# Performance work log

Hardware: AMD Instinct MI355X
Metric: run time of the kernel (lower is better)

## Reference

```python
import jax, jax.numpy as jnp
import numpy as np

EPS_GN = 1e-8
EPS_ATTN = 1e-8


def setup_inputs() -> dict:
    key = jax.random.key(0)
    ks = jax.random.split(key, 13)
    B, C, N = 4, 512, 2048
    s = 0.02
    return {
        "x": jax.random.normal(ks[0], (B, C, N), jnp.float32),
        "dw_w": jax.random.normal(ks[1], (C, 3), jnp.float32) * s,
        "pw_w": jax.random.normal(ks[2], (C, C), jnp.float32) * s,
        "u_w": jax.random.normal(ks[3], (2 * C, C), jnp.float32) * s,
        "u_b": jax.random.normal(ks[4], (2 * C,), jnp.float32) * s,
        "v_w": jax.random.normal(ks[5], (2 * C, C), jnp.float32) * s,
        "v_b": jax.random.normal(ks[6], (2 * C,), jnp.float32) * s,
        "h_w": jax.random.normal(ks[7], (C, C), jnp.float32) * s,
        "h_b": jax.random.normal(ks[8], (C,), jnp.float32) * s,
        "q_w": jax.random.normal(ks[9], (C, C), jnp.float32) * s,
        "k_w": jax.random.normal(ks[10], (C, C), jnp.float32) * s,
        "o_w": jax.random.normal(ks[11], (C, 2 * C), jnp.float32) * s,
        "o_b": jax.random.normal(ks[12], (C,), jnp.float32) * s,
    }


def reference(x, dw_w, pw_w, u_w, u_b, v_w, v_b, h_w, h_b, q_w, k_w, o_w, o_b):
    # x: [B, C, N]
    C = x.shape[1]
    # GroupNorm(1, C): normalize over (C, N) per sample; affine is identity-init
    # in torch but we follow the module math with default weight=1, bias=0
    mean = jnp.mean(x, axis=(1, 2), keepdims=True)
    var = jnp.var(x, axis=(1, 2), keepdims=True)
    z = (x - mean) * jax.lax.rsqrt(var + EPS_GN)

    # local depthwise conv k=3, pad=1 (cross-correlation), no bias
    zp = jnp.pad(z, ((0, 0), (0, 0), (1, 1)))
    dw = (dw_w[:, 0, None] * zp[:, :, :-2]
          + dw_w[:, 1, None] * zp[:, :, 1:-1]
          + dw_w[:, 2, None] * zp[:, :, 2:])
    # pointwise conv (no bias)
    z = z + jnp.einsum('oc,bcn->bon', pw_w, dw)

    u = jax.nn.sigmoid(jnp.einsum('oc,bcn->bon', u_w, z) + u_b[:, None])  # [B,2C,N]
    v = jnp.einsum('oc,bcn->bon', v_w, z) + v_b[:, None]                  # [B,2C,N]
    h = jnp.einsum('oc,bcn->bno', h_w, z) + h_b                           # [B,N,C]

    q = h @ q_w.T  # [B,N,C]
    k = h @ k_w.T  # [B,N,C]
    scale = 1.0 / jnp.sqrt(jnp.float32(C))

    logits = jnp.einsum('bnc,bmc->bnm', q, k) * scale
    a = jax.nn.relu(logits)
    a = a * a
    a = a / (jnp.sum(a, axis=-1, keepdims=True) + EPS_ATTN)

    av = jnp.einsum('bnm,bom->bon', a, v)  # [B,2C,N]
    y = jnp.einsum('oc,bcn->bon', o_w, u * av) + o_b[:, None]
    return x + y
```

## Files before the change

### kernel.cpp

```cpp
#include <hip/hip_runtime.h>
#include <hip/hip_bf16.h>
#include <cstdint>

typedef __bf16 bhalf;
typedef __bf16 bhalf8 __attribute__((ext_vector_type(8)));
typedef float f32x4 __attribute__((ext_vector_type(4)));

enum { EPI_Z2=0, EPI_UV=1, EPI_BIAS=2, EPI_QK=3, EPI_ATTN=4, EPI_PV=5, EPI_Y=6, EPI_ST=7 };

__device__ __forceinline__ void gl_lds16(const void* g, void* l) {
  __builtin_amdgcn_global_load_lds(
      (const __attribute__((address_space(1))) unsigned int*)g,
      (__attribute__((address_space(3))) unsigned int*)l,
      16, 0, 0);
}
__device__ __forceinline__ void barrier_raw() { asm volatile("s_barrier" ::: "memory"); }
#define VMW(n)  asm volatile("s_waitcnt vmcnt(" #n ")" ::: "memory")
#define LGKM0() asm volatile("s_waitcnt lgkmcnt(0)" ::: "memory")

__device__ __forceinline__ unsigned char to_fp8(float v){
  return (unsigned char)(__builtin_amdgcn_cvt_pk_fp8_f32(v, v, 0, false) & 0xff);
}


template<int EPI>
__global__ void __launch_bounds__(512, 2)
gA(const bhalf* __restrict__ A, const bhalf* __restrict__ Bw,
   void* __restrict__ Out, void* __restrict__ Out2,
   const float* __restrict__ bias, const float* __restrict__ bias2,
   int N, int K, long sA, long sB, long sO, long sAuxf, float scale)
{
  constexpr int KSL = 256*64;
  constexpr int REG = 2*KSL;
  constexpr int DBUF = 2*REG;
  __shared__ __align__(16) char lds[2*DBUF];

  const int gx = gridDim.x, gy = gridDim.y;
  const int nwg = gx*gy;
  const int flat = blockIdx.y*gx + blockIdx.x;
  const int q8 = nwg>>3, r8 = nwg&7, xcd = flat&7, o8 = flat>>3;
  const int wsw = (xcd<r8 ? xcd*(q8+1) : r8*(q8+1)+(xcd-r8)*q8) + o8;
  const int bx = wsw % gx, by = wsw / gx;
  const int m0 = by*256, n0 = bx*256;
  const int bz = blockIdx.z;

  const bhalf* Ab = A + (long)bz*sA;
  const bhalf* Bb = Bw + (long)bz*sB;

  const int tid = threadIdx.x, wid = tid>>6, lane = tid&63;
  const int lm = lane&15, kq = lane>>4;
  const int wm = wid>>2, wn = wid&3;
  const int srow = lane>>2;
  const int csw = ((lane&3) ^ ((lane>>3)&3)) * 8;
  const int kqs = kq ^ ((lm>>1)&3);

  f32x4 acc[8][4];
  #pragma unroll
  for (int i=0;i<8;i++)
    #pragma unroll
    for (int j=0;j<4;j++) acc[i][j] = f32x4{0.f,0.f,0.f,0.f};

  auto stageA = [&](int kt){
    char* base = lds + (kt&1)*DBUF;
    const int k0 = kt*64;
    #pragma unroll
    for (int h=0; h<2; h++)
      #pragma unroll
      for (int ksl=0; ksl<2; ksl++){
        bhalf* d = (bhalf*)(base + ksl*KSL + (h*128 + wid*16)*64);
        gl_lds16(Ab + (long)(m0 + h*128 + wid*16 + srow)*K + k0 + ksl*32 + csw, d);
      }
  };
  auto stageB = [&](int kt){
    char* base = lds + (kt&1)*DBUF + REG;
    const int k0 = kt*64;
    #pragma unroll
    for (int h=0; h<2; h++)
      #pragma unroll
      for (int ksl=0; ksl<2; ksl++){
        bhalf* d = (bhalf*)(base + ksl*KSL + (h*128 + wid*16)*64);
        gl_lds16(Bb + (long)(n0 + h*128 + wid*16 + srow)*K + k0 + ksl*32 + csw, d);
      }
  };

  bhalf8 af[4][2], bf[4][2];
  auto readA = [&](int kt, int ih){
    char* base = lds + (kt&1)*DBUF;
    #pragma unroll
    for (int i2=0;i2<4;i2++)
      #pragma unroll
      for (int ksl=0;ksl<2;ksl++)
        af[i2][ksl] = *(const bhalf8*)(base + ksl*KSL + (wm*128 + ih*64 + i2*16 + lm)*64 + kqs*16);
  };
  auto readB = [&](int kt, int jh){
    char* base = lds + (kt&1)*DBUF + REG;
    #pragma unroll
    for (int j2=0;j2<2;j2++)
      #pragma unroll
      for (int ksl=0;ksl<2;ksl++)
        bf[jh*2+j2][ksl] = *(const bhalf8*)(base + ksl*KSL + (wn*64 + jh*32 + j2*16 + lm)*64 + kqs*16);
  };
  auto mfma16 = [&](int ih, int jh){
    __builtin_amdgcn_s_setprio(1);
    #pragma unroll
    for (int i2=0;i2<4;i2++)
      #pragma unroll
      for (int j2=0;j2<2;j2++)
        #pragma unroll
        for (int ksl=0;ksl<2;ksl++)
          acc[ih*4+i2][jh*2+j2] = __builtin_amdgcn_mfma_f32_16x16x32_bf16(
              af[i2][ksl], bf[jh*2+j2][ksl], acc[ih*4+i2][jh*2+j2], 0,0,0);
    __builtin_amdgcn_s_setprio(0);
  };

  const int NT = K>>6;
  stageA(0); stageB(0); stageA(1);
  for (int kt=0; kt<NT; ++kt){
    if (kt==NT-1) { VMW(0); } else { VMW(4); }
    barrier_raw();
    readA(kt,0); readB(kt,0);
    if (kt+1<NT) stageB(kt+1);
    mfma16(0,0);
    barrier_raw();
    readB(kt,1);
    mfma16(0,1);
    barrier_raw();
    readA(kt,1);
    mfma16(1,0);
    barrier_raw();
    if (kt+2<NT) stageA(kt+2);
    mfma16(1,1);
  }
  barrier_raw();

  if constexpr (EPI==EPI_UV){
    const bool uh = n0 < 1024;
    const float* bv = uh ? bias : bias2;
    const int bc0 = uh ? n0 : n0-1024;
    #pragma unroll
    for (int i=0;i<8;i++){
      #pragma unroll
      for (int j=0;j<4;j++){
        const int lcol = wn*64 + j*16 + lm;
        #pragma unroll
        for (int r=0;r<4;r++){
          const int lrow = wm*128 + i*16 + kq*4 + r;
          float v = acc[i][j][r] + bv[bc0 + lcol];
          if (uh){
            v = 1.f/(1.f + __expf(-v));
            const int cb = lcol*2;
            const int lb = lrow*512 + (((cb>>5) ^ ((lrow>>2)&3))<<5) + (cb&31);
            *(bhalf*)(lds + lb) = (bhalf)v;
          } else {
            const int lb = lcol*256 + ((((lrow>>4) ^ (lcol&15)))<<4) + (lrow&15);
            *(unsigned char*)(lds + lb) = to_fp8(v);
          }
        }
      }
    }
    LGKM0();
    barrier_raw();
    if (uh){
      char* obase = (char*)Out + 2*((long)m0*1024 + n0);
      #pragma unroll
      for (int it=0; it<16; ++it){
        const int g = (it*512 + tid)*16;
        const int row = g >> 9, off = g & 511;
        const int lb = row*512 + (((off>>5) ^ ((row>>2)&3))<<5) + (off&31);
        uint4 val = *(const uint4*)(lds + lb);
        *(uint4*)(obase + (long)row*2048 + off) = val;
      }
    } else {
      char* vb = (char*)Out2 + ((long)(m0>>11)*1024*2048 + (long)(n0-1024)*2048 + (m0 & 2047));
      #pragma unroll
      for (int it=0; it<8; ++it){
        const int g = (it*512 + tid)*16;
        const int row = g >> 8, off = g & 255;
        const int lb = row*256 + ((((off>>4) ^ (row&15)))<<4);
        uint4 val = *(const uint4*)(lds + lb);
        *(uint4*)(vb + (long)row*2048 + off) = val;
      }
    }
  }
  (void)scale; (void)bias; (void)bias2; (void)N; (void)sO; (void)sAuxf;
}

__global__ void __launch_bounds__(256, 2)
gsc8(const unsigned char* __restrict__ Q, const unsigned char* __restrict__ Kp,
     unsigned char* __restrict__ Wsc, float* __restrict__ rden, float scale)
{
  constexpr int DBUF = 256*64;
  __shared__ __align__(16) char lds[3*DBUF];

  const int gx = gridDim.x, gy = gridDim.y;
  const int nwg = gx*gy;
  const int flat = blockIdx.y*gx + blockIdx.x;
  const int q8 = nwg>>3, r8 = nwg&7, xcd = flat&7, o8 = flat>>3;
  const int w = (xcd<r8 ? xcd*(q8+1) : r8*(q8+1)+(xcd-r8)*q8) + o8;
  const int bx = w % gx, by = w / gx;
  const int m0 = by*128, n0 = bx*128;
  const int bz = blockIdx.z;
  const int K = 512;

  const unsigned char* Ab = Q  + (long)bz*2048*512;
  const unsigned char* Bb = Kp + (long)bz*2048*512;

  const int tid = threadIdx.x;
  const int wid = tid>>6, lane = tid&63;
  const int lm = lane&15, kq = lane>>4;
  const int wm = wid>>1, wn = wid&1;
  const int srow = lane>>2;
  const int csw8 = ((lane&3) ^ ((lane>>3)&3))*16;
  int coff[2];
  #pragma unroll
  for (int ksl=0; ksl<2; ksl++)
    coff[ksl] = ((((ksl*2 + (kq>>1)) ^ ((lm>>1)&3)))<<4) + ((kq&1)<<3);

  f32x4 acc[4][4];
  #pragma unroll
  for (int i=0;i<4;i++)
    #pragma unroll
    for (int j=0;j<4;j++) acc[i][j] = f32x4{0.f,0.f,0.f,0.f};

  auto stage = [&](int kt){
    char* base = lds + (kt%3)*DBUF;
    const int k0 = kt*64;
    #pragma unroll
    for (int c=0;c<4;c++){
      const int r0 = c*64 + wid*16;
      char* d = base + r0*64;
      const unsigned char* g = (r0 < 128)
        ? Ab + (long)(m0 + r0 + srow)*K + k0 + csw8
        : Bb + (long)(n0 + r0 - 128 + srow)*K + k0 + csw8;
      gl_lds16(g, d);
    }
  };

  long af[4][2], bf[4][2];
  auto readA = [&](int kt){
    char* base = lds + (kt%3)*DBUF;
    #pragma unroll
    for (int i2=0;i2<4;i2++)
      #pragma unroll
      for (int ksl=0;ksl<2;ksl++)
        af[i2][ksl] = *(const long*)(base + (wm*64 + i2*16 + lm)*64 + coff[ksl]);
  };
  auto readB = [&](int kt, int jh){
    char* base = lds + (kt%3)*DBUF;
    #pragma unroll
    for (int j2=0;j2<2;j2++)
      #pragma unroll
      for (int ksl=0;ksl<2;ksl++)
        bf[jh*2+j2][ksl] = *(const long*)(base + (128 + wn*64 + jh*32 + j2*16 + lm)*64 + coff[ksl]);
  };
  auto mfma16 = [&](int jh){
    __builtin_amdgcn_s_setprio(1);
    #pragma unroll
    for (int i2=0;i2<4;i2++)
      #pragma unroll
      for (int j2=0;j2<2;j2++)
        #pragma unroll
        for (int ksl=0;ksl<2;ksl++)
          acc[i2][jh*2+j2] = __builtin_amdgcn_mfma_f32_16x16x32_fp8_fp8(
              af[i2][ksl], bf[jh*2+j2][ksl], acc[i2][jh*2+j2], 0,0,0);
    __builtin_amdgcn_s_setprio(0);
  };

  const int NT = 8;
  stage(0); stage(1);
  for (int kt=0; kt<NT; ++kt){
    if (kt==NT-1) { VMW(0); } else { VMW(4); }
    barrier_raw();
    readA(kt); readB(kt,0);
    if (kt+2<NT) stage(kt+2);
    mfma16(0);
    readB(kt,1);
    mfma16(1);
  }
  barrier_raw();

  float rs[4][4];
  #pragma unroll
  for (int i=0;i<4;i++)
    #pragma unroll
    for (int r=0;r<4;r++) rs[i][r]=0.f;
  #pragma unroll
  for (int i=0;i<4;i++){
    #pragma unroll
    for (int j=0;j<4;j++){
      const int lcol = wn*64 + j*16 + lm;
      #pragma unroll
      for (int r=0;r<4;r++){
        const int lrow = wm*64 + i*16 + kq*4 + r;
        float v = acc[i][j][r];
        v *= scale; v = fmaxf(v,0.f); v = v*v;
        rs[i][r] += v;
        const int lb = lrow*128 + ((((lcol>>4) ^ (lrow&7)))<<4) + (lcol&15);
        *(unsigned char*)(lds + lb) = to_fp8(v);
      }
    }
  }
  float* rd = rden + (long)bz*2048;
  #pragma unroll
  for (int i=0;i<4;i++){
    const int rbase = m0 + wm*64 + i*16 + kq*4;
    #pragma unroll
    for (int r=0;r<4;r++){
      float s = rs[i][r];
      s += __shfl_xor(s,1); s += __shfl_xor(s,2);
      s += __shfl_xor(s,4); s += __shfl_xor(s,8);
      if (lm==0) atomicAdd(rd + rbase + r, s);
    }
  }
  LGKM0();
  barrier_raw();
  unsigned char* obase = Wsc + (long)bz*2048*2048 + (long)m0*2048 + n0;
  #pragma unroll
  for (int it=0; it<4; ++it){
    const int g = (it*256 + tid)*16;
    const int row = g >> 7, off = g & 127;
    const int lb = row*128 + ((((off>>4) ^ (row&7)))<<4);
    uint4 val = *(const uint4*)(lds + lb);
    *(uint4*)(obase + (long)row*2048 + off) = val;
  }
}

__global__ void __launch_bounds__(256, 2)
g4k8(const unsigned char* __restrict__ A, const unsigned char* __restrict__ Bw,
     bhalf* __restrict__ Out,
     const bhalf* __restrict__ ub, const float* __restrict__ rden,
     int K, long sB, int rowshift)
{
  constexpr int DBUF = 256*64;
  __shared__ __align__(16) char lds[4*DBUF];

  const int gx = gridDim.x, gy = gridDim.y;
  const int nwg = gx*gy;
  const int flat = blockIdx.y*gx + blockIdx.x;
  const int q8 = nwg>>3, r8 = nwg&7, xcd = flat&7, o8 = flat>>3;
  const int w = (xcd<r8 ? xcd*(q8+1) : r8*(q8+1)+(xcd-r8)*q8) + o8;
  const int bx = w % gx, by = w / gx;
  const int m0 = by*128, n0 = bx*128;

  const unsigned char* Bb = Bw + (long)(m0>>rowshift)*sB;

  const int tid = threadIdx.x;
  const int wid = tid>>6, lane = tid&63;
  const int lm = lane&15, kq = lane>>4;
  const int wm = wid>>1, wn = wid&1;
  const int srow = lane>>2;
  const int csw8 = ((lane&3) ^ ((lane>>3)&3))*16;
  int coff[2];
  #pragma unroll
  for (int ksl=0; ksl<2; ksl++)
    coff[ksl] = ((((ksl*2 + (kq>>1)) ^ ((lm>>1)&3)))<<4) + ((kq&1)<<3);

  f32x4 acc[4][4];
  #pragma unroll
  for (int i=0;i<4;i++)
    #pragma unroll
    for (int j=0;j<4;j++) acc[i][j] = f32x4{0.f,0.f,0.f,0.f};

  auto stage = [&](int kt){
    char* base = lds + (kt&3)*DBUF;
    const int k0 = kt*64;
    #pragma unroll
    for (int c=0;c<4;c++){
      const int r0 = c*64 + wid*16;
      char* d = base + r0*64;
      const unsigned char* g = (r0 < 128)
        ? A  + (long)(m0 + r0 + srow)*K + k0 + csw8
        : Bb + (long)(n0 + r0 - 128 + srow)*K + k0 + csw8;
      gl_lds16(g, d);
    }
  };

  long af[4][2], bf[4][2];
  auto readA = [&](int kt){
    char* base = lds + (kt&3)*DBUF;
    #pragma unroll
    for (int i2=0;i2<4;i2++)
      #pragma unroll
      for (int ksl=0;ksl<2;ksl++)
        af[i2][ksl] = *(const long*)(base + (wm*64 + i2*16 + lm)*64 + coff[ksl]);
  };
  auto readB = [&](int kt, int jh){
    char* base = lds + (kt&3)*DBUF;
    #pragma unroll
    for (int j2=0;j2<2;j2++)
      #pragma unroll
      for (int ksl=0;ksl<2;ksl++)
        bf[jh*2+j2][ksl] = *(const long*)(base + (128 + wn*64 + jh*32 + j2*16 + lm)*64 + coff[ksl]);
  };
  auto mfma16 = [&](int jh){
    __builtin_amdgcn_s_setprio(1);
    #pragma unroll
    for (int i2=0;i2<4;i2++)
      #pragma unroll
      for (int j2=0;j2<2;j2++)
        #pragma unroll
        for (int ksl=0;ksl<2;ksl++)
          acc[i2][jh*2+j2] = __builtin_amdgcn_mfma_f32_16x16x32_fp8_fp8(
              af[i2][ksl], bf[jh*2+j2][ksl], acc[i2][jh*2+j2], 0,0,0);
    __builtin_amdgcn_s_setprio(0);
  };

  const int NT = K>>6;
  stage(0); stage(1); stage(2);
  for (int kt=0; kt<NT; ++kt){
    if (kt==NT-1)      { VMW(0); }
    else if (kt==NT-2) { VMW(4); }
    else               { VMW(8); }
    barrier_raw();
    readA(kt); readB(kt,0);
    if (kt+3<NT) stage(kt+3);
    mfma16(0);
    readB(kt,1);
    mfma16(1);
  }
  barrier_raw();

  char* obase = (char*)Out + 2*((long)m0*1024 + n0);
  #pragma unroll
  for (int i=0;i<4;i++){
    #pragma unroll
    for (int j=0;j<4;j++){
      const int lcol = wn*64 + j*16 + lm;
      #pragma unroll
      for (int r=0;r<4;r++){
        const int lrow = wm*64 + i*16 + kq*4 + r;
        const int rowg = m0 + lrow;
        float v = acc[i][j][r];
        float den = rden[rowg];
        v *= __builtin_amdgcn_rcpf(den + 1e-8f);
        v *= (float)ub[(long)rowg*1024 + n0 + lcol];
        const int cb = lcol*2;
        const int lb = lrow*256 + (((cb>>5) ^ ((lrow>>2)&3))<<5) + (cb&31);
        *(bhalf*)(lds + lb) = (bhalf)v;
      }
    }
  }
  LGKM0();
  barrier_raw();
  #pragma unroll
  for (int it=0; it<8; ++it){
    const int g = (it*256 + tid)*16;
    const int row = g >> 8, off = g & 255;
    const int lb = row*256 + (((off>>5) ^ ((row>>2)&3))<<5) + (off&31);
    uint4 val = *(const uint4*)(lds + lb);
    *(uint4*)(obase + (long)row*2048 + off) = val;
  }
}

template<int EPI>
__global__ void __launch_bounds__(256, 2)
g4k(const bhalf* __restrict__ A, const bhalf* __restrict__ Bw,
    void* __restrict__ Out, void* __restrict__ Out2,
    const float* __restrict__ bias,
    const bhalf* __restrict__ auxb,
    const float* __restrict__ xadd,
    int M, int N, int K)
{
  constexpr int KSL = 256*64;
  constexpr int DBUF = 2*KSL;
  __shared__ __align__(16) char lds[2*DBUF];

  const int gx = gridDim.x, gy = gridDim.y;
  const int nwg = gx*gy;
  const int flat = blockIdx.y*gx + blockIdx.x;
  const int q8 = nwg>>3, r8 = nwg&7, xcd = flat&7, o8 = flat>>3;
  const int w = (xcd<r8 ? xcd*(q8+1) : r8*(q8+1)+(xcd-r8)*q8) + o8;
  const int bx = w % gx, by = w / gx;
  const int m0 = by*128, n0 = bx*128;

  const int tid = threadIdx.x;
  const int wid = tid>>6, lane = tid&63;
  const int lm = lane&15, kq = lane>>4;
  const int wm = wid>>1, wn = wid&1;
  const int srow = lane>>2;
  const int csw = ((lane&3) ^ ((lane>>3)&3))*8;
  const int kqs = kq ^ ((lm>>1)&3);

  f32x4 acc[4][4];
  #pragma unroll
  for (int i=0;i<4;i++)
    #pragma unroll
    for (int j=0;j<4;j++) acc[i][j] = f32x4{0.f,0.f,0.f,0.f};

  auto stage = [&](int kt){
    char* base = lds + (kt&1)*DBUF;
    const int k0 = kt*64;
    #pragma unroll
    for (int c=0;c<4;c++){
      const int r0 = c*64 + wid*16;
      #pragma unroll
      for (int ksl=0; ksl<2; ksl++){
        bhalf* d = (bhalf*)(base + ksl*KSL + r0*64);
        const bhalf* g = (r0 < 128)
          ? A  + (long)(m0 + r0 + srow)*K + k0 + ksl*32 + csw
          : Bw + (long)(n0 + r0 - 128 + srow)*K + k0 + ksl*32 + csw;
        gl_lds16(g, d);
      }
    }
  };

  bhalf8 af[4][2], bf[4][2];
  auto readA = [&](int kt){
    char* base = lds + (kt&1)*DBUF;
    #pragma unroll
    for (int i2=0;i2<4;i2++)
      #pragma unroll
      for (int ksl=0;ksl<2;ksl++)
        af[i2][ksl] = *(const bhalf8*)(base + ksl*KSL + (wm*64 + i2*16 + lm)*64 + kqs*16);
  };
  auto readB = [&](int kt, int jh){
    char* base = lds + (kt&1)*DBUF;
    #pragma unroll
    for (int j2=0;j2<2;j2++)
      #pragma unroll
      for (int ksl=0;ksl<2;ksl++)
        bf[jh*2+j2][ksl] = *(const bhalf8*)(base + ksl*KSL + (128 + wn*64 + jh*32 + j2*16 + lm)*64 + kqs*16);
  };
  auto mfma16 = [&](int jh){
    __builtin_amdgcn_s_setprio(1);
    #pragma unroll
    for (int i2=0;i2<4;i2++)
      #pragma unroll
      for (int j2=0;j2<2;j2++)
        #pragma unroll
        for (int ksl=0;ksl<2;ksl++)
          acc[i2][jh*2+j2] = __builtin_amdgcn_mfma_f32_16x16x32_bf16(
              af[i2][ksl], bf[jh*2+j2][ksl], acc[i2][jh*2+j2], 0,0,0);
    __builtin_amdgcn_s_setprio(0);
  };

  const int NT = K>>6;
  stage(0); stage(1);
  for (int kt=0; kt<NT; ++kt){
    if (kt==NT-1) { VMW(0); } else { VMW(8); }
    barrier_raw();
    readA(kt); readB(kt,0);
    mfma16(0);
    barrier_raw();
    readB(kt,1);
    if (kt+2<NT) stage(kt+2);
    mfma16(1);
  }
  barrier_raw();

  if constexpr (EPI==EPI_Y){
    #pragma unroll
    for (int i=0;i<4;i++){
      #pragma unroll
      for (int j=0;j<4;j++){
        const int lcol = wn*64 + j*16 + lm;
        #pragma unroll
        for (int r=0;r<4;r++){
          const int lrow = wm*64 + i*16 + kq*4 + r;
          float v = acc[i][j][r] + bias[n0 + lcol];
          const int lb = lcol*512 + 4*(lrow ^ ((lcol&15)<<2));
          *(float*)(lds + lb) = v;
        }
      }
    }
    LGKM0();
    barrier_raw();
    const int b = m0 >> 11, nb = m0 & 2047;
    float* ob = (float*)Out + ((long)b*512 + n0)*2048 + nb;
    const float* xb = xadd + ((long)b*512 + n0)*2048 + nb;
    #pragma unroll
    for (int it=0; it<16; ++it){
      const int g = (it*256 + tid)*16;
      const int row = g >> 9, off = g & 511;
      const int t0 = off >> 2;
      const int s = (row&15)<<2;
      f32x4 vv = *(const f32x4*)(lds + row*512 + 4*(t0^s));
      f32x4 xx = *(const f32x4*)(xb + (long)row*2048 + t0);
      *(f32x4*)(ob + (long)row*2048 + t0) = vv + xx;
    }
  } else if constexpr (EPI==EPI_QK){
    bool qh = n0 < 512;
    unsigned char* obase = (unsigned char*)(qh?Out:Out2) + (long)m0*512 + (n0 - (qh?0:512));
    #pragma unroll
    for (int i=0;i<4;i++){
      #pragma unroll
      for (int j=0;j<4;j++){
        const int lcol = wn*64 + j*16 + lm;
        #pragma unroll
        for (int r=0;r<4;r++){
          const int lrow = wm*64 + i*16 + kq*4 + r;
          float v = acc[i][j][r] + bias[n0 + lcol];
          const int lb = lrow*128 + ((((lcol>>4) ^ (lrow&7)))<<4) + (lcol&15);
          *(unsigned char*)(lds + lb) = to_fp8(v);
        }
      }
    }
    LGKM0();
    barrier_raw();
    #pragma unroll
    for (int it=0; it<4; ++it){
      const int g = (it*256 + tid)*16;
      const int row = g >> 7, off = g & 127;
      const int lb = row*128 + ((((off>>4) ^ (row&7)))<<4);
      uint4 val = *(const uint4*)(lds + lb);
      *(uint4*)(obase + (long)row*512 + off) = val;
    }
  } else {
    char* obase = (char*)Out + 2*((long)m0*N + n0);
    const int ldb = N*2;
    #pragma unroll
    for (int i=0;i<4;i++){
      #pragma unroll
      for (int j=0;j<4;j++){
        const int lcol = wn*64 + j*16 + lm;
        #pragma unroll
        for (int r=0;r<4;r++){
          const int lrow = wm*64 + i*16 + kq*4 + r;
          float v = acc[i][j][r];
          if constexpr (EPI==EPI_Z2)
            v += (float)auxb[(long)(m0+lrow)*N + n0 + lcol];
          if constexpr (EPI==EPI_BIAS)
            v += bias[n0 + lcol];
          const int cb = lcol*2;
          const int lb = lrow*256 + (((cb>>5) ^ ((lrow>>2)&3))<<5) + (cb&31);
          *(bhalf*)(lds + lb) = (bhalf)v;
        }
      }
    }
    LGKM0();
    barrier_raw();
    #pragma unroll
    for (int it=0; it<8; ++it){
      const int g = (it*256 + tid)*16;
      const int row = g >> 8, off = g & 255;
      const int lb = row*256 + (((off>>5) ^ ((row>>2)&3))<<5) + (off&31);
      uint4 val = *(const uint4*)(lds + lb);
      *(uint4*)(obase + (long)row*ldb + off) = val;
    }
  }
  (void)M; (void)xadd; (void)bias; (void)auxb;
}

struct CvtArgs { const float* src[7]; bhalf* dst[7]; int n[7]; };
__global__ void cvt_multi(CvtArgs a) {
  int seg = blockIdx.y;
  int i = (blockIdx.x*256 + threadIdx.x)*4;
  if (i >= a.n[seg]) return;
  float4 f = *(const float4*)(a.src[seg] + i);
  bhalf* d = a.dst[seg] + i;
  d[0]=(bhalf)f.x; d[1]=(bhalf)f.y; d[2]=(bhalf)f.z; d[3]=(bhalf)f.w;
}

__global__ void transpose_bf16(const bhalf* __restrict__ in, bhalf* __restrict__ out,
                               int R, int C) {
  __shared__ bhalf t[32][33];
  int r0 = blockIdx.x*32, c0 = blockIdx.y*32;
  int tx = threadIdx.x, ty = threadIdx.y;
  #pragma unroll
  for (int r=0;r<4;r++)
    t[ty + r*8][tx] = in[(long)(r0 + ty + r*8)*C + c0 + tx];
  __syncthreads();
  #pragma unroll
  for (int r=0;r<4;r++)
    out[(long)(c0 + ty + r*8)*R + r0 + tx] = t[tx][ty + r*8];
}

__global__ void qk_bias(const bhalf* __restrict__ wqk, const float* __restrict__ hb,
                        float* __restrict__ bq){
  int row = blockIdx.x*4 + (threadIdx.x>>6);
  int lane = threadIdx.x & 63;
  const bhalf* p = wqk + (long)row*512;
  float s = 0.f;
  #pragma unroll
  for (int j=0;j<8;j++) s += (float)p[lane*8+j] * hb[lane*8+j];
  for (int off=32; off; off>>=1) s += __shfl_xor(s, off);
  if (lane==0) bq[row] = s;
}

__global__ void gn_part(const float* __restrict__ x, float* __restrict__ ps, float* __restrict__ pss) {
  int b = blockIdx.y;
  const float* xb = x + (long)b*(512*2048);
  float s=0.f, ss=0.f;
  #pragma unroll
  for (int it=0; it<8; it++){
    int idx = ((it*128 + blockIdx.x)*256 + threadIdx.x)*4;
    float4 f = *(const float4*)(xb + idx);
    s  += f.x+f.y+f.z+f.w;
    ss += f.x*f.x+f.y*f.y+f.z*f.z+f.w*f.w;
  }
  for (int off=32; off; off>>=1){ s += __shfl_xor(s,off); ss += __shfl_xor(ss,off); }
  __shared__ float ls[4], lss[4];
  int wid = threadIdx.x>>6, lane = threadIdx.x&63;
  if (lane==0){ ls[wid]=s; lss[wid]=ss; }
  __syncthreads();
  if (threadIdx.x==0){
    s = ls[0]+ls[1]+ls[2]+ls[3]; ss = lss[0]+lss[1]+lss[2]+lss[3];
    ps[b*128 + blockIdx.x] = s; pss[b*128 + blockIdx.x] = ss;
  }
}

__global__ void gn_final(const float* __restrict__ ps, const float* __restrict__ pss,
                         float* __restrict__ stats) {
  int b = blockIdx.x;
  float s = ps[b*128 + threadIdx.x], ss = pss[b*128 + threadIdx.x];
  for (int off=32; off; off>>=1){ s += __shfl_xor(s,off); ss += __shfl_xor(ss,off); }
  __shared__ float l0[2], l1[2];
  int wid = threadIdx.x>>6, lane = threadIdx.x&63;
  if (lane==0){ l0[wid]=s; l1[wid]=ss; }
  __syncthreads();
  if (threadIdx.x==0){
    s = l0[0]+l0[1]; ss = l1[0]+l1[1];
    float mean = s*(1.f/1048576.f);
    float var  = ss*(1.f/1048576.f) - mean*mean;
    stats[b*2] = mean; stats[b*2+1] = rsqrtf(var + 1e-8f);
  }
}

__global__ void norm_dw_T(const float* __restrict__ x, const float* __restrict__ stats,
                          const float* __restrict__ dw_w,
                          bhalf* __restrict__ zT, bhalf* __restrict__ dwT) {
  int b = blockIdx.z, n0 = blockIdx.x*32, c0 = blockIdx.y*32;
  float mean = stats[b*2], rstd = stats[b*2+1];
  __shared__ float zs[32][35];
  int tx = threadIdx.x, ty = threadIdx.y;
  #pragma unroll
  for (int r=0;r<4;r++){
    int c = c0 + ty + r*8;
    for (int cc=tx; cc<34; cc+=32){
      int n = n0 - 1 + cc;
      float v = 0.f;
      if (n>=0 && n<2048) v = (x[((long)b*512 + c)*2048 + n] - mean)*rstd;
      zs[ty + r*8][cc] = v;
    }
  }
  __syncthreads();
  float w0 = dw_w[(c0+tx)*3+0], w1 = dw_w[(c0+tx)*3+1], w2 = dw_w[(c0+tx)*3+2];
  #pragma unroll
  for (int r=0;r<4;r++){
    int ln = ty + r*8;
    float z = zs[tx][ln+1];
    float d = w0*zs[tx][ln] + w1*zs[tx][ln+1] + w2*zs[tx][ln+2];
    long o = ((long)b*2048 + n0 + ln)*512 + c0 + tx;
    zT[o] = (bhalf)z; dwT[o] = (bhalf)d;
  }
}

extern "C" void kernel_launch(void* const* d_in, const int* in_sizes, int n_in,
                              void* d_out, int out_size, void* d_ws, size_t ws_size,
                              hipStream_t stream) {
  (void)in_sizes; (void)n_in; (void)out_size; (void)ws_size;
  const float* x    = (const float*)d_in[0];
  const float* dw_w = (const float*)d_in[1];
  const float* pw_w = (const float*)d_in[2];
  const float* u_w  = (const float*)d_in[3];
  const float* u_b  = (const float*)d_in[4];
  const float* v_w  = (const float*)d_in[5];
  const float* v_b  = (const float*)d_in[6];
  const float* h_w  = (const float*)d_in[7];
  const float* h_b  = (const float*)d_in[8];
  const float* q_w  = (const float*)d_in[9];
  const float* k_w  = (const float*)d_in[10];
  const float* o_w  = (const float*)d_in[11];
  const float* o_b  = (const float*)d_in[12];
  float* out = (float*)d_out;

  char* ws = (char*)d_ws;
  size_t off = 0;
  auto alloc = [&](size_t bytes) -> void* {
    void* p = ws + off; off = (off + bytes + 255) & ~(size_t)255; return p;
  };

  float* ps    = (float*)alloc(4*128*4);
  float* pss   = (float*)alloc(4*128*4);
  float* stats = (float*)alloc(4*2*4);
  float* rden  = (float*)alloc(4*2048*4);
  float* bq    = (float*)alloc(1024*4);
  bhalf* wb_pw = (bhalf*)alloc(512*512*2);
  bhalf* wb_uv = (bhalf*)alloc((size_t)2048*512*2);
  bhalf* wb_h  = (bhalf*)alloc(512*512*2);
  bhalf* hwT   = (bhalf*)alloc(512*512*2);
  bhalf* wb_qk = (bhalf*)alloc((size_t)1024*512*2);
  bhalf* wqk2  = (bhalf*)alloc((size_t)1024*512*2);
  bhalf* wb_o  = (bhalf*)alloc((size_t)512*1024*2);
  const size_t ACT = (size_t)4*2048*512;
  bhalf* zT   = (bhalf*)alloc(ACT*2);
  bhalf* dwT  = (bhalf*)alloc(ACT*2);
  bhalf* z2T  = (bhalf*)alloc(ACT*2);
  bhalf* ub   = (bhalf*)alloc(ACT*2*2);
  unsigned char* v_fm = (unsigned char*)alloc((size_t)4*1024*2048);
  unsigned char* wsc  = (unsigned char*)alloc((size_t)4*2048*2048);
  unsigned char* qb8  = (unsigned char*)alloc(ACT);
  unsigned char* kb8  = (unsigned char*)alloc(ACT);
  bhalf* uav  = (bhalf*)alloc(ACT*2*2);

  hipMemsetAsync(rden, 0, 4*2048*4, stream);

  CvtArgs ca;
  ca.src[0]=pw_w; ca.dst[0]=wb_pw;           ca.n[0]=512*512;
  ca.src[1]=u_w;  ca.dst[1]=wb_uv;           ca.n[1]=1024*512;
  ca.src[2]=v_w;  ca.dst[2]=wb_uv+1024*512;  ca.n[2]=1024*512;
  ca.src[3]=h_w;  ca.dst[3]=wb_h;            ca.n[3]=512*512;
  ca.src[4]=q_w;  ca.dst[4]=wb_qk;           ca.n[4]=512*512;
  ca.src[5]=k_w;  ca.dst[5]=wb_qk+512*512;   ca.n[5]=512*512;
  ca.src[6]=o_w;  ca.dst[6]=wb_o;            ca.n[6]=512*1024;
  cvt_multi<<<dim3(512,7), 256, 0, stream>>>(ca);

  transpose_bf16<<<dim3(16,16), dim3(32,8), 0, stream>>>(wb_h, hwT, 512, 512);
  g4k<EPI_ST><<<dim3(4,8,1), 256, 0, stream>>>(wb_qk, hwT, wqk2, nullptr,
      nullptr, nullptr, nullptr, 1024, 512, 512);
  qk_bias<<<dim3(256), 256, 0, stream>>>(wb_qk, h_b, bq);

  gn_part<<<dim3(128,4), 256, 0, stream>>>(x, ps, pss);
  gn_final<<<dim3(4), 128, 0, stream>>>(ps, pss, stats);

  norm_dw_T<<<dim3(64,16,4), dim3(32,8), 0, stream>>>(x, stats, dw_w, zT, dwT);

  const float iscl = 0.044194173824159216f;
  g4k<EPI_Z2><<<dim3(4,64,1), 256, 0, stream>>>(dwT, wb_pw, z2T, nullptr,
      nullptr, zT, nullptr, 8192, 512, 512);
  gA<EPI_UV><<<dim3(8,32,1), 512, 0, stream>>>(z2T, wb_uv, ub, v_fm,
      u_b, v_b, 2048, 512, 0, 0, 0, 0, 0.f);
  g4k<EPI_QK><<<dim3(8,64,1), 256, 0, stream>>>(z2T, wqk2, qb8, kb8,
      bq, nullptr, nullptr, 8192, 1024, 512);
  gsc8<<<dim3(16,16,4), 256, 0, stream>>>(qb8, kb8, wsc, rden, iscl);
  g4k8<<<dim3(8,64,1), 256, 0, stream>>>(wsc, v_fm, uav, ub, rden,
      2048, (long)1024*2048, 11);
  g4k<EPI_Y><<<dim3(4,64,1), 256, 0, stream>>>(uav, wb_o, out, nullptr,
      o_b, nullptr, x, 8192, 512, 1024);
}
```

Baseline: 176.3 us.

## Compute U/V projection GEMM in FP8 with fused FP8 z2 output

```diff
diff --git a/kernel.cpp b/kernel.cpp
--- a/kernel.cpp
+++ b/kernel.cpp
@@ -6,7 +6,7 @@
 typedef __bf16 bhalf8 __attribute__((ext_vector_type(8)));
 typedef float f32x4 __attribute__((ext_vector_type(4)));
 
-enum { EPI_Z2=0, EPI_UV=1, EPI_BIAS=2, EPI_QK=3, EPI_ATTN=4, EPI_PV=5, EPI_Y=6, EPI_ST=7 };
+enum { EPI_Z2=0, EPI_BIAS=2, EPI_QK=3, EPI_Y=6, EPI_ST=7 };
 
 __device__ __forceinline__ void gl_lds16(const void* g, void* l) {
   __builtin_amdgcn_global_load_lds(
@@ -22,168 +22,6 @@
   return (unsigned char)(__builtin_amdgcn_cvt_pk_fp8_f32(v, v, 0, false) & 0xff);
 }
 
-
-template<int EPI>
-__global__ void __launch_bounds__(512, 2)
-gA(const bhalf* __restrict__ A, const bhalf* __restrict__ Bw,
-   void* __restrict__ Out, void* __restrict__ Out2,
-   const float* __restrict__ bias, const float* __restrict__ bias2,
-   int N, int K, long sA, long sB, long sO, long sAuxf, float scale)
-{
-  constexpr int KSL = 256*64;
-  constexpr int REG = 2*KSL;
-  constexpr int DBUF = 2*REG;
-  __shared__ __align__(16) char lds[2*DBUF];
-
-  const int gx = gridDim.x, gy = gridDim.y;
-  const int nwg = gx*gy;
-  const int flat = blockIdx.y*gx + blockIdx.x;
-  const int q8 = nwg>>3, r8 = nwg&7, xcd = flat&7, o8 = flat>>3;
-  const int wsw = (xcd<r8 ? xcd*(q8+1) : r8*(q8+1)+(xcd-r8)*q8) + o8;
-  const int bx = wsw % gx, by = wsw / gx;
-  const int m0 = by*256, n0 = bx*256;
-  const int bz = blockIdx.z;
-
-  const bhalf* Ab = A + (long)bz*sA;
-  const bhalf* Bb = Bw + (long)bz*sB;
-
-  const int tid = threadIdx.x, wid = tid>>6, lane = tid&63;
-  const int lm = lane&15, kq = lane>>4;
-  const int wm = wid>>2, wn = wid&3;
-  const int srow = lane>>2;
-  const int csw = ((lane&3) ^ ((lane>>3)&3)) * 8;
-  const int kqs = kq ^ ((lm>>1)&3);
-
-  f32x4 acc[8][4];
-  #pragma unroll
-  for (int i=0;i<8;i++)
-    #pragma unroll
-    for (int j=0;j<4;j++) acc[i][j] = f32x4{0.f,0.f,0.f,0.f};
-
-  auto stageA = [&](int kt){
-    char* base = lds + (kt&1)*DBUF;
-    const int k0 = kt*64;
-    #pragma unroll
-    for (int h=0; h<2; h++)
-      #pragma unroll
-      for (int ksl=0; ksl<2; ksl++){
-        bhalf* d = (bhalf*)(base + ksl*KSL + (h*128 + wid*16)*64);
-        gl_lds16(Ab + (long)(m0 + h*128 + wid*16 + srow)*K + k0 + ksl*32 + csw, d);
-      }
-  };
-  auto stageB = [&](int kt){
-    char* base = lds + (kt&1)*DBUF + REG;
-    const int k0 = kt*64;
-    #pragma unroll
-    for (int h=0; h<2; h++)
-      #pragma unroll
-      for (int ksl=0; ksl<2; ksl++){
-        bhalf* d = (bhalf*)(base + ksl*KSL + (h*128 + wid*16)*64);
-        gl_lds16(Bb + (long)(n0 + h*128 + wid*16 + srow)*K + k0 + ksl*32 + csw, d);
-      }
-  };
-
-  bhalf8 af[4][2], bf[4][2];
-  auto readA = [&](int kt, int ih){
-    char* base = lds + (kt&1)*DBUF;
-    #pragma unroll
-    for (int i2=0;i2<4;i2++)
-      #pragma unroll
-      for (int ksl=0;ksl<2;ksl++)
-        af[i2][ksl] = *(const bhalf8*)(base + ksl*KSL + (wm*128 + ih*64 + i2*16 + lm)*64 + kqs*16);
-  };
-  auto readB = [&](int kt, int jh){
-    char* base = lds + (kt&1)*DBUF + REG;
-    #pragma unroll
-    for (int j2=0;j2<2;j2++)
-      #pragma unroll
-      for (int ksl=0;ksl<2;ksl++)
-        bf[jh*2+j2][ksl] = *(const bhalf8*)(base + ksl*KSL + (wn*64 + jh*32 + j2*16 + lm)*64 + kqs*16);
-  };
-  auto mfma16 = [&](int ih, int jh){
-    __builtin_amdgcn_s_setprio(1);
-    #pragma unroll
-    for (int i2=0;i2<4;i2++)
-      #pragma unroll
-      for (int j2=0;j2<2;j2++)
-        #pragma unroll
-        for (int ksl=0;ksl<2;ksl++)
-          acc[ih*4+i2][jh*2+j2] = __builtin_amdgcn_mfma_f32_16x16x32_bf16(
-              af[i2][ksl], bf[jh*2+j2][ksl], acc[ih*4+i2][jh*2+j2], 0,0,0);
-    __builtin_amdgcn_s_setprio(0);
-  };
-
-  const int NT = K>>6;
-  stageA(0); stageB(0); stageA(1);
-  for (int kt=0; kt<NT; ++kt){
-    if (kt==NT-1) { VMW(0); } else { VMW(4); }
-    barrier_raw();
-    readA(kt,0); readB(kt,0);
-    if (kt+1<NT) stageB(kt+1);
-    mfma16(0,0);
-    barrier_raw();
-    readB(kt,1);
-    mfma16(0,1);
-    barrier_raw();
-    readA(kt,1);
-    mfma16(1,0);
-    barrier_raw();
-    if (kt+2<NT) stageA(kt+2);
-    mfma16(1,1);
-  }
-  barrier_raw();
-
-  if constexpr (EPI==EPI_UV){
-    const bool uh = n0 < 1024;
-    const float* bv = uh ? bias : bias2;
-    const int bc0 = uh ? n0 : n0-1024;
-    #pragma unroll
-    for (int i=0;i<8;i++){
-      #pragma unroll
-      for (int j=0;j<4;j++){
-        const int lcol = wn*64 + j*16 + lm;
-        #pragma unroll
-        for (int r=0;r<4;r++){
-          const int lrow = wm*128 + i*16 + kq*4 + r;
-          float v = acc[i][j][r] + bv[bc0 + lcol];
-          if (uh){
-            v = 1.f/(1.f + __expf(-v));
-            const int cb = lcol*2;
-            const int lb = lrow*512 + (((cb>>5) ^ ((lrow>>2)&3))<<5) + (cb&31);
-            *(bhalf*)(lds + lb) = (bhalf)v;
-          } else {
-            const int lb = lcol*256 + ((((lrow>>4) ^ (lcol&15)))<<4) + (lrow&15);
-            *(unsigned char*)(lds + lb) = to_fp8(v);
-          }
-        }
-      }
-    }
-    LGKM0();
-    barrier_raw();
-    if (uh){
-      char* obase = (char*)Out + 2*((long)m0*1024 + n0);
-      #pragma unroll
-      for (int it=0; it<16; ++it){
-        const int g = (it*512 + tid)*16;
-        const int row = g >> 9, off = g & 511;
-        const int lb = row*512 + (((off>>5) ^ ((row>>2)&3))<<5) + (off&31);
-        uint4 val = *(const uint4*)(lds + lb);
-        *(uint4*)(obase + (long)row*2048 + off) = val;
-      }
-    } else {
-      char* vb = (char*)Out2 + ((long)(m0>>11)*1024*2048 + (long)(n0-1024)*2048 + (m0 & 2047));
-      #pragma unroll
-      for (int it=0; it<8; ++it){
-        const int g = (it*512 + tid)*16;
-        const int row = g >> 8, off = g & 255;
-        const int lb = row*256 + ((((off>>4) ^ (row&15)))<<4);
-        uint4 val = *(const uint4*)(lds + lb);
-        *(uint4*)(vb + (long)row*2048 + off) = val;
-      }
-    }
-  }
-  (void)scale; (void)bias; (void)bias2; (void)N; (void)sO; (void)sAuxf;
-}
 
 __global__ void __launch_bounds__(256, 2)
 gsc8(const unsigned char* __restrict__ Q, const unsigned char* __restrict__ Kp,
@@ -322,6 +160,155 @@
     const int lb = row*128 + ((((off>>4) ^ (row&7)))<<4);
     uint4 val = *(const uint4*)(lds + lb);
     *(uint4*)(obase + (long)row*2048 + off) = val;
+  }
+}
+
+__global__ void __launch_bounds__(256, 2)
+guv8(const unsigned char* __restrict__ A, const unsigned char* __restrict__ Bw,
+     bhalf* __restrict__ Ub, unsigned char* __restrict__ Vfm,
+     const float* __restrict__ ubias, const float* __restrict__ vbias)
+{
+  constexpr int DBUF = 256*64;
+  __shared__ __align__(16) char lds[3*DBUF];
+
+  const int gx = gridDim.x, gy = gridDim.y;
+  const int nwg = gx*gy;
+  const int flat = blockIdx.y*gx + blockIdx.x;
+  const int q8 = nwg>>3, r8 = nwg&7, xcd = flat&7, o8 = flat>>3;
+  const int w = (xcd<r8 ? xcd*(q8+1) : r8*(q8+1)+(xcd-r8)*q8) + o8;
+  const int bx = w % gx, by = w / gx;
+  const int m0 = by*128, n0 = bx*128;
+  const int K = 512;
+
+  const int tid = threadIdx.x;
+  const int wid = tid>>6, lane = tid&63;
+  const int lm = lane&15, kq = lane>>4;
+  const int wm = wid>>1, wn = wid&1;
+  const int srow = lane>>2;
+  const int csw8 = ((lane&3) ^ ((lane>>3)&3))*16;
+  int coff[2];
+  #pragma unroll
+  for (int ksl=0; ksl<2; ksl++)
+    coff[ksl] = ((((ksl*2 + (kq>>1)) ^ ((lm>>1)&3)))<<4) + ((kq&1)<<3);
+
+  f32x4 acc[4][4];
+  #pragma unroll
+  for (int i=0;i<4;i++)
+    #pragma unroll
+    for (int j=0;j<4;j++) acc[i][j] = f32x4{0.f,0.f,0.f,0.f};
+
+  auto stage = [&](int kt){
+    char* base = lds + (kt%3)*DBUF;
+    const int k0 = kt*64;
+    #pragma unroll
+    for (int c=0;c<4;c++){
+      const int r0 = c*64 + wid*16;
+      char* d = base + r0*64;
+      const unsigned char* g = (r0 < 128)
+        ? A  + (long)(m0 + r0 + srow)*K + k0 + csw8
+        : Bw + (long)(n0 + r0 - 128 + srow)*K + k0 + csw8;
+      gl_lds16(g, d);
+    }
+  };
+
+  long af[4][2], bf[4][2];
+  auto readA = [&](int kt){
+    char* base = lds + (kt%3)*DBUF;
+    #pragma unroll
+    for (int i2=0;i2<4;i2++)
+      #pragma unroll
+      for (int ksl=0;ksl<2;ksl++)
+        af[i2][ksl] = *(const long*)(base + (wm*64 + i2*16 + lm)*64 + coff[ksl]);
+  };
+  auto readB = [&](int kt, int jh){
+    char* base = lds + (kt%3)*DBUF;
+    #pragma unroll
+    for (int j2=0;j2<2;j2++)
+      #pragma unroll
+      for (int ksl=0;ksl<2;ksl++)
+        bf[jh*2+j2][ksl] = *(const long*)(base + (128 + wn*64 + jh*32 + j2*16 + lm)*64 + coff[ksl]);
+  };
+  auto mfma16 = [&](int jh){
+    __builtin_amdgcn_s_setprio(1);
+    #pragma unroll
+    for (int i2=0;i2<4;i2++)
+      #pragma unroll
+      for (int j2=0;j2<2;j2++)
+        #pragma unroll
+        for (int ksl=0;ksl<2;ksl++)
+          acc[i2][jh*2+j2] = __builtin_amdgcn_mfma_f32_16x16x32_fp8_fp8(
+              af[i2][ksl], bf[jh*2+j2][ksl], acc[i2][jh*2+j2], 0,0,0);
+    __builtin_amdgcn_s_setprio(0);
+  };
+
+  const int NT = 8;
+  stage(0); stage(1);
+  for (int kt=0; kt<NT; ++kt){
+    if (kt==NT-1) { VMW(0); } else { VMW(4); }
+    barrier_raw();
+    readA(kt); readB(kt,0);
+    if (kt+2<NT) stage(kt+2);
+    mfma16(0);
+    readB(kt,1);
+    mfma16(1);
+  }
+  barrier_raw();
+
+  const bool uh = n0 < 1024;
+  if (uh){
+    #pragma unroll
+    for (int i=0;i<4;i++){
+      #pragma unroll
+      for (int j=0;j<4;j++){
+        const int lcol = wn*64 + j*16 + lm;
+        #pragma unroll
+        for (int r=0;r<4;r++){
+          const int lrow = wm*64 + i*16 + kq*4 + r;
+          float v = acc[i][j][r] + ubias[n0 + lcol];
+          v = 1.f/(1.f + __expf(-v));
+          const int cb = lcol*2;
+          const int lb = lrow*256 + (((cb>>5) ^ ((lrow>>2)&3))<<5) + (cb&31);
+          *(bhalf*)(lds + lb) = (bhalf)v;
+        }
+      }
+    }
+    LGKM0();
+    barrier_raw();
+    char* obase = (char*)Ub + 2*((long)m0*1024 + n0);
+    #pragma unroll
+    for (int it=0; it<8; ++it){
+      const int g = (it*256 + tid)*16;
+      const int row = g >> 8, off = g & 255;
+      const int lb = row*256 + (((off>>5) ^ ((row>>2)&3))<<5) + (off&31);
+      uint4 val = *(const uint4*)(lds + lb);
+      *(uint4*)(obase + (long)row*2048 + off) = val;
+    }
+  } else {
+    #pragma unroll
+    for (int i=0;i<4;i++){
+      #pragma unroll
+      for (int j=0;j<4;j++){
+        const int lcol = wn*64 + j*16 + lm;
+        #pragma unroll
+        for (int r=0;r<4;r++){
+          const int lrow = wm*64 + i*16 + kq*4 + r;
+          float v = acc[i][j][r] + vbias[n0 - 1024 + lcol];
+          const int lb = lcol*128 + ((((lrow>>4) ^ (lcol&7)))<<4) + (lrow&15);
+          *(unsigned char*)(lds + lb) = to_fp8(v);
+        }
+      }
+    }
+    LGKM0();
+    barrier_raw();
+    unsigned char* vb = Vfm + ((long)(m0>>11)*1024*2048 + (long)(n0-1024)*2048 + (m0 & 2047));
+    #pragma unroll
+    for (int it=0; it<4; ++it){
+      const int g = (it*256 + tid)*16;
+      const int row = g >> 7, off = g & 127;
+      const int lb = row*128 + ((((off>>4) ^ (row&7)))<<4);
+      uint4 val = *(const uint4*)(lds + lb);
+      *(uint4*)(vb + (long)row*2048 + off) = val;
+    }
   }
 }
 
@@ -624,6 +611,10 @@
           const int cb = lcol*2;
           const int lb = lrow*256 + (((cb>>5) ^ ((lrow>>2)&3))<<5) + (cb&31);
           *(bhalf*)(lds + lb) = (bhalf)v;
+          if constexpr (EPI==EPI_Z2){
+            const int lb2 = 32768 + lrow*128 + ((((lcol>>4) ^ (lrow&7)))<<4) + (lcol&15);
+            *(unsigned char*)(lds + lb2) = to_fp8(v);
+          }
         }
       }
     }
@@ -637,11 +628,22 @@
       uint4 val = *(const uint4*)(lds + lb);
       *(uint4*)(obase + (long)row*ldb + off) = val;
     }
+    if constexpr (EPI==EPI_Z2){
+      unsigned char* o8 = (unsigned char*)Out2 + (long)m0*N + n0;
+      #pragma unroll
+      for (int it=0; it<4; ++it){
+        const int g = (it*256 + tid)*16;
+        const int row = g >> 7, off = g & 127;
+        const int lb = 32768 + row*128 + ((((off>>4) ^ (row&7)))<<4);
+        uint4 val = *(const uint4*)(lds + lb);
+        *(uint4*)(o8 + (long)row*N + off) = val;
+      }
+    }
   }
   (void)M; (void)xadd; (void)bias; (void)auxb;
 }
 
-struct CvtArgs { const float* src[7]; bhalf* dst[7]; int n[7]; };
+struct CvtArgs { const float* src[5]; bhalf* dst[5]; int n[5]; };
 __global__ void cvt_multi(CvtArgs a) {
   int seg = blockIdx.y;
   int i = (blockIdx.x*256 + threadIdx.x)*4;
@@ -649,6 +651,14 @@
   float4 f = *(const float4*)(a.src[seg] + i);
   bhalf* d = a.dst[seg] + i;
   d[0]=(bhalf)f.x; d[1]=(bhalf)f.y; d[2]=(bhalf)f.z; d[3]=(bhalf)f.w;
+}
+
+__global__ void cvt_fp8(const float* __restrict__ src, unsigned char* __restrict__ dst, int n){
+  int i = (blockIdx.x*256 + threadIdx.x)*4;
+  if (i >= n) return;
+  float4 f = *(const float4*)(src + i);
+  dst[i+0]=to_fp8(f.x); dst[i+1]=to_fp8(f.y);
+  dst[i+2]=to_fp8(f.z); dst[i+3]=to_fp8(f.w);
 }
 
 __global__ void transpose_bf16(const bhalf* __restrict__ in, bhalf* __restrict__ out,
@@ -776,7 +786,7 @@
   float* rden  = (float*)alloc(4*2048*4);
   float* bq    = (float*)alloc(1024*4);
   bhalf* wb_pw = (bhalf*)alloc(512*512*2);
-  bhalf* wb_uv = (bhalf*)alloc((size_t)2048*512*2);
+  unsigned char* wuv8 = (unsigned char*)alloc((size_t)2048*512);
   bhalf* wb_h  = (bhalf*)alloc(512*512*2);
   bhalf* hwT   = (bhalf*)alloc(512*512*2);
   bhalf* wb_qk = (bhalf*)alloc((size_t)1024*512*2);
@@ -786,6 +796,7 @@
   bhalf* zT   = (bhalf*)alloc(ACT*2);
   bhalf* dwT  = (bhalf*)alloc(ACT*2);
   bhalf* z2T  = (bhalf*)alloc(ACT*2);
+  unsigned char* z2f8 = (unsigned char*)alloc(ACT);
   bhalf* ub   = (bhalf*)alloc(ACT*2*2);
   unsigned char* v_fm = (unsigned char*)alloc((size_t)4*1024*2048);
   unsigned char* wsc  = (unsigned char*)alloc((size_t)4*2048*2048);
@@ -797,13 +808,13 @@
 
   CvtArgs ca;
   ca.src[0]=pw_w; ca.dst[0]=wb_pw;           ca.n[0]=512*512;
-  ca.src[1]=u_w;  ca.dst[1]=wb_uv;           ca.n[1]=1024*512;
-  ca.src[2]=v_w;  ca.dst[2]=wb_uv+1024*512;  ca.n[2]=1024*512;
-  ca.src[3]=h_w;  ca.dst[3]=wb_h;            ca.n[3]=512*512;
-  ca.src[4]=q_w;  ca.dst[4]=wb_qk;           ca.n[4]=512*512;
-  ca.src[5]=k_w;  ca.dst[5]=wb_qk+512*512;   ca.n[5]=512*512;
-  ca.src[6]=o_w;  ca.dst[6]=wb_o;            ca.n[6]=512*1024;
-  cvt_multi<<<dim3(512,7), 256, 0, stream>>>(ca);
+  ca.src[1]=h_w;  ca.dst[1]=wb_h;            ca.n[1]=512*512;
+  ca.src[2]=q_w;  ca.dst[2]=wb_qk;           ca.n[2]=512*512;
+  ca.src[3]=k_w;  ca.dst[3]=wb_qk+512*512;   ca.n[3]=512*512;
+  ca.src[4]=o_w;  ca.dst[4]=wb_o;            ca.n[4]=512*1024;
+  cvt_multi<<<dim3(512,5), 256, 0, stream>>>(ca);
+  cvt_fp8<<<dim3(512), 256, 0, stream>>>(u_w, wuv8,          1024*512);
+  cvt_fp8<<<dim3(512), 256, 0, stream>>>(v_w, wuv8+1024*512, 1024*512);
 
   transpose_bf16<<<dim3(16,16), dim3(32,8), 0, stream>>>(wb_h, hwT, 512, 512);
   g4k<EPI_ST><<<dim3(4,8,1), 256, 0, stream>>>(wb_qk, hwT, wqk2, nullptr,
@@ -816,10 +827,9 @@
   norm_dw_T<<<dim3(64,16,4), dim3(32,8), 0, stream>>>(x, stats, dw_w, zT, dwT);
 
   const float iscl = 0.044194173824159216f;
-  g4k<EPI_Z2><<<dim3(4,64,1), 256, 0, stream>>>(dwT, wb_pw, z2T, nullptr,
+  g4k<EPI_Z2><<<dim3(4,64,1), 256, 0, stream>>>(dwT, wb_pw, z2T, z2f8,
       nullptr, zT, nullptr, 8192, 512, 512);
-  gA<EPI_UV><<<dim3(8,32,1), 512, 0, stream>>>(z2T, wb_uv, ub, v_fm,
-      u_b, v_b, 2048, 512, 0, 0, 0, 0, 0.f);
+  guv8<<<dim3(16,64,1), 256, 0, stream>>>(z2f8, wuv8, ub, v_fm, u_b, v_b);
   g4k<EPI_QK><<<dim3(8,64,1), 256, 0, stream>>>(z2T, wqk2, qb8, kb8,
       bq, nullptr, nullptr, 8192, 1024, 512);
   gsc8<<<dim3(16,16,4), 256, 0, stream>>>(qb8, kb8, wsc, rden, iscl);
```

Result: no change. 172.8 us (-2.0%).
